# Optimization experiments

Measured on AMD Instinct MI355X. Metric: run time of the kernel, lower is better.

Reference implementation:

```python
import jax, jax.numpy as jnp
import numpy as np

NQ = 4
PI_HALF = np.pi / 2
HAD = jnp.array([[1, 1], [1, -1]], dtype=jnp.complex64) / np.sqrt(2)
CNOT = jnp.array([[1, 0, 0, 0], [0, 1, 0, 0], [0, 0, 0, 1], [0, 0, 1, 0]], dtype=jnp.complex64)
_bits = (np.arange(2 ** NQ)[:, None] >> np.arange(NQ - 1, -1, -1)[None, :]) & 1
ZSIGNS = jnp.asarray(1.0 - 2.0 * _bits, jnp.float32)  # [16, NQ]


def _ry(theta):
    c = jnp.cos(theta / 2).astype(jnp.complex64)
    s = jnp.sin(theta / 2).astype(jnp.complex64)
    return jnp.stack([jnp.stack([c, -s], -1), jnp.stack([s, c], -1)], -2)  # [...,2,2]


def _rot(phi, theta, omega):
    # PennyLane Rot = RZ(omega) @ RY(theta) @ RZ(phi)
    c = jnp.cos(theta / 2).astype(jnp.complex64)
    s = jnp.sin(theta / 2).astype(jnp.complex64)
    ep = jnp.exp(0.5j * phi).astype(jnp.complex64)
    eo = jnp.exp(0.5j * omega).astype(jnp.complex64)
    return jnp.stack([jnp.stack([jnp.conj(ep) * jnp.conj(eo) * c, -ep * jnp.conj(eo) * s]),
                      jnp.stack([jnp.conj(ep) * eo * s, ep * eo * c])])


def _cry(theta):
    # controlled-RY, batched: [B] -> [B,4,4], basis order (control, target)
    B = theta.shape[0]
    U = jnp.zeros((B, 4, 4), jnp.complex64).at[:, 0, 0].set(1.0).at[:, 1, 1].set(1.0)
    return U.at[:, 2:, 2:].set(_ry(theta))


def _apply1(state, U, wire):
    s = jnp.moveaxis(state, wire + 1, 1)
    shp = s.shape
    s = s.reshape(shp[0], 2, -1)
    s = jnp.einsum('ij,bjk->bik', U, s) if U.ndim == 2 else jnp.einsum('bij,bjk->bik', U, s)
    return jnp.moveaxis(s.reshape(shp), 1, wire + 1)


def _apply2(state, U, q0, q1):
    s = jnp.moveaxis(state, (q0 + 1, q1 + 1), (1, 2))
    shp = s.shape
    s = s.reshape(shp[0], 4, -1)
    s = jnp.einsum('ij,bjk->bik', U, s) if U.ndim == 2 else jnp.einsum('bij,bjk->bik', U, s)
    return jnp.moveaxis(s.reshape(shp), (1, 2), (q0 + 1, q1 + 1))


def _init_state(B):
    s = jnp.zeros((B, 2 ** NQ), jnp.complex64).at[:, 0].set(1.0)
    return s.reshape((B,) + (2,) * NQ)


def _zexp(state):
    p = state.reshape(state.shape[0], -1)
    p = p.real ** 2 + p.imag ** 2
    return p @ ZSIGNS  # [B, NQ]


def _attention_circuit(q, k, params):
    # q, k: [E, NQ] angles; params: [NQ, 3] shared
    s = _init_state(q.shape[0])
    for i in range(NQ):
        s = _apply1(s, _ry(q[:, i]), i)
    for i in range(NQ):
        s = _apply1(s, HAD, i)
    for i in range(NQ):
        s = _apply2(s, _cry(k[:, i]), i, (i + 1) % NQ)
    for i in range(NQ):
        s = _apply1(s, _rot(params[i, 0], params[i, 1], params[i, 2]), i)
    return _zexp(s)


def _entangle_circuit(x, params):
    # x: [N, NQ] angles; params: [n_layers, NQ, 3]
    s = _init_state(x.shape[0])
    for i in range(NQ):
        s = _apply1(s, _ry(x[:, i]), i)
    for l in range(params.shape[0]):
        for i in range(NQ - 1):
            s = _apply2(s, CNOT, i, i + 1)
        for i in range(NQ):
            s = _apply1(s, _rot(params[l, i, 0], params[l, i, 1], params[l, i, 2]), i)
        s = _apply2(s, CNOT, 0, NQ - 1)  # n_qubits >= 4
    return _zexp(s)


def _path_circuit(x, params):
    # x: [N, NQ]; params: [3, NQ, 3]
    s = _init_state(x.shape[0])
    for i in range(NQ):
        s = _apply1(s, HAD, i)
    for i in range(NQ):
        s = _apply1(s, _ry(x[:, i]), i)
    for l in range(3):
        for i in range(NQ):
            s = _apply1(s, _rot(params[l, i, 0], params[l, i, 1], params[l, i, 2]), i)
        for i in range(NQ - 1):
            s = _apply2(s, CNOT, i, i + 1)
    return _zexp(s)


def _forward(x, W_in, b_in, lin_W, lin_b, qproj_W, qproj_b, ent_params,
             attq_W, attq_b, attk_W, attk_b, att_qp, path_params,
             path_in_W, path_in_b, path_out_W, path_out_b, out_W, out_b, edge_index):
    N = x.shape[0]
    loops = jnp.arange(N, dtype=edge_index.dtype)
    ei = jnp.concatenate([edge_index, jnp.stack([loops, loops])], axis=1)  # add_self_loops
    src, dst = ei[0], ei[1]
    h = jax.nn.relu(x @ W_in.T + b_in)
    for l in range(lin_W.shape[0]):
        x_cls = h @ lin_W[l].T + lin_b[l]
        xq = _entangle_circuit(jnp.tanh(h[:, :NQ]) * PI_HALF, ent_params[l])
        x_comb = x_cls + xq @ qproj_W[l].T + qproj_b[l]
        q = jnp.tanh(h @ attq_W[l].T + attq_b[l]) * PI_HALF
        k = jnp.tanh(h @ attk_W[l].T + attk_b[l]) * PI_HALF
        scores = _attention_circuit(q[src], k[dst], att_qp[l]).mean(axis=1)  # [E]
        att = jax.nn.softmax(scores)  # global softmax over all edges (faithful)
        h = jax.ops.segment_sum(att[:, None] * x_comb[src], dst, num_segments=N)
        h = jax.nn.relu(h)  # dropout is identity at eval
    pq = jnp.tanh(h @ path_in_W.T + path_in_b) * PI_HALF
    h = _path_circuit(pq, path_params) @ path_out_W.T + path_out_b
    return h @ out_W.T + out_b


def setup_inputs() -> dict:
    key = jax.random.key(0)
    ks = jax.random.split(key, 22)
    N, E, D_in, D_h, D_out, L = 20000, 300000, 64, 128, 32, 2
    w = lambda k, shape: jax.random.normal(k, shape, jnp.float32) * 0.1
    return {
        'x': jax.random.normal(ks[0], (N, D_in), jnp.float32),
        'W_in': w(ks[1], (D_h, D_in)), 'b_in': w(ks[2], (D_h,)),
        'lin_W': w(ks[3], (L, D_h, D_h)), 'lin_b': w(ks[4], (L, D_h)),
        'qproj_W': w(ks[5], (L, D_h, NQ)), 'qproj_b': w(ks[6], (L, D_h)),
        'ent_params': w(ks[7], (L, 2, NQ, 3)),
        'attq_W': w(ks[8], (L, NQ, D_h)), 'attq_b': w(ks[9], (L, NQ)),
        'attk_W': w(ks[10], (L, NQ, D_h)), 'attk_b': w(ks[11], (L, NQ)),
        'att_qp': w(ks[12], (L, NQ, 3)),
        'path_params': w(ks[13], (3, NQ, 3)),
        'path_in_W': w(ks[14], (NQ, D_h)), 'path_in_b': w(ks[15], (NQ,)),
        'path_out_W': w(ks[16], (D_h, NQ)), 'path_out_b': w(ks[17], (D_h,)),
        'out_W': w(ks[18], (D_out, D_h)), 'out_b': w(ks[19], (D_out,)),
        'edge_index': jax.random.randint(ks[20], (2, E), 0, N, dtype=jnp.int32),
    }


def reference(x, W_in, b_in, lin_W, lin_b, qproj_W, qproj_b, ent_params,
              attq_W, attq_b, attk_W, attk_b, att_qp, path_params,
              path_in_W, path_in_b, path_out_W, path_out_b, out_W, out_b, edge_index):
    return _forward(x, W_in, b_in, lin_W, lin_b, qproj_W, qproj_b, ent_params,
                    attq_W, attq_b, attk_W, attk_b, att_qp, path_params,
                    path_in_W, path_in_b, path_out_W, path_out_b, out_W, out_b, edge_index)
```

## Files before the change

kernel.cpp:

```cpp
#include <hip/hip_runtime.h>
#include <math.h>

#define PI_HALF 1.57079632679489662f


__device__ __forceinline__ void init_state(float sr[16], float si[16]) {
#pragma unroll
    for (int i = 0; i < 16; ++i) { sr[i] = 0.f; si[i] = 0.f; }
    sr[0] = 1.f;
}

template<int M>
__device__ __forceinline__ void ry_g(float sr[16], float si[16], float c, float s) {
#pragma unroll
    for (int i = 0; i < 16; ++i) {
        if (i & M) continue;
        const int j = i | M;
        float ar = sr[i], ai = si[i], br = sr[j], bi = si[j];
        sr[i] = c * ar - s * br;  si[i] = c * ai - s * bi;
        sr[j] = s * ar + c * br;  si[j] = s * ai + c * bi;
    }
}

template<int M>
__device__ __forceinline__ void had_g(float sr[16], float si[16]) {
    const float r = 0.70710678118654752f;
#pragma unroll
    for (int i = 0; i < 16; ++i) {
        if (i & M) continue;
        const int j = i | M;
        float ar = sr[i], ai = si[i], br = sr[j], bi = si[j];
        sr[i] = (ar + br) * r;  si[i] = (ai + bi) * r;
        sr[j] = (ar - br) * r;  si[j] = (ai - bi) * r;
    }
}

template<int MC, int MT>
__device__ __forceinline__ void cnot_g(float sr[16], float si[16]) {
#pragma unroll
    for (int i = 0; i < 16; ++i) {
        if (!(i & MC) || (i & MT)) continue;
        const int j = i | MT;
        float tr = sr[i], ti = si[i];
        sr[i] = sr[j]; si[i] = si[j];
        sr[j] = tr;    si[j] = ti;
    }
}

template<int MC, int MT>
__device__ __forceinline__ void cry_g(float sr[16], float si[16], float c, float s) {
#pragma unroll
    for (int i = 0; i < 16; ++i) {
        if (!(i & MC) || (i & MT)) continue;
        const int j = i | MT;
        float ar = sr[i], ai = si[i], br = sr[j], bi = si[j];
        sr[i] = c * ar - s * br;  si[i] = c * ai - s * bi;
        sr[j] = s * ar + c * br;  si[j] = s * ai + c * bi;
    }
}

template<int M>
__device__ __forceinline__ void rot_g(float sr[16], float si[16],
                                      float phi, float theta, float omega) {
    float st, ct; sincosf(0.5f * theta, &st, &ct);
    float sp, cp; sincosf(0.5f * (phi + omega), &sp, &cp);
    float sm, cm; sincosf(0.5f * (phi - omega), &sm, &cm);
    float u00r =  ct * cp, u00i = -ct * sp;
    float u01r = -st * cm, u01i = -st * sm;
    float u10r =  st * cm, u10i = -st * sm;
    float u11r =  ct * cp, u11i =  ct * sp;
#pragma unroll
    for (int i = 0; i < 16; ++i) {
        if (i & M) continue;
        const int j = i | M;
        float ar = sr[i], ai = si[i], br = sr[j], bi = si[j];
        sr[i] = u00r * ar - u00i * ai + u01r * br - u01i * bi;
        si[i] = u00r * ai + u00i * ar + u01r * bi + u01i * br;
        sr[j] = u10r * ar - u10i * ai + u11r * br - u11i * bi;
        si[j] = u10r * ai + u10i * ar + u11r * bi + u11i * br;
    }
}

__device__ __forceinline__ void zexp_g(const float sr[16], const float si[16], float z[4]) {
    float p[16];
#pragma unroll
    for (int i = 0; i < 16; ++i) p[i] = sr[i] * sr[i] + si[i] * si[i];
    z[0] = z[1] = z[2] = z[3] = 0.f;
#pragma unroll
    for (int i = 0; i < 16; ++i) {
        z[0] += (i & 8) ? -p[i] : p[i];
        z[1] += (i & 4) ? -p[i] : p[i];
        z[2] += (i & 2) ? -p[i] : p[i];
        z[3] += (i & 1) ? -p[i] : p[i];
    }
}


__global__ void k_in(const float* __restrict__ x, const float* __restrict__ W,
                     const float* __restrict__ b, float* __restrict__ h, int N) {
    __shared__ float xs[16 * 64];
    const int base = blockIdx.x * 16;
    const int tid = threadIdx.x;
    for (int idx = tid; idx < 16 * 64; idx += 128) {
        int n = base + (idx >> 6);
        xs[idx] = (n < N) ? x[(size_t)n * 64 + (idx & 63)] : 0.f;
    }
    __syncthreads();
    float acc[16];
#pragma unroll
    for (int n = 0; n < 16; ++n) acc[n] = 0.f;
    const float4* wr4 = (const float4*)(W + tid * 64);
    for (int c4 = 0; c4 < 16; ++c4) {
        float4 w = wr4[c4];
#pragma unroll
        for (int n = 0; n < 16; ++n) {
            float4 hv = *(const float4*)&xs[n * 64 + c4 * 4];
            acc[n] += w.x * hv.x + w.y * hv.y + w.z * hv.z + w.w * hv.w;
        }
    }
    const float bb = b[tid];
#pragma unroll
    for (int n = 0; n < 16; ++n) {
        int node = base + n;
        if (node < N) h[(size_t)node * 128 + tid] = fmaxf(acc[n] + bb, 0.f);
    }
}

__global__ void k_ent(const float* __restrict__ h, const float* __restrict__ ep,
                      float* __restrict__ xq, int N) {
    int n = blockIdx.x * blockDim.x + threadIdx.x;
    if (n >= N) return;
    float4 hv = *(const float4*)&h[(size_t)n * 128];
    float a[4] = { tanhf(hv.x) * PI_HALF, tanhf(hv.y) * PI_HALF,
                   tanhf(hv.z) * PI_HALF, tanhf(hv.w) * PI_HALF };
    float sr[16], si[16];
    init_state(sr, si);
    { float s, c; sincosf(0.5f * a[0], &s, &c); ry_g<8>(sr, si, c, s); }
    { float s, c; sincosf(0.5f * a[1], &s, &c); ry_g<4>(sr, si, c, s); }
    { float s, c; sincosf(0.5f * a[2], &s, &c); ry_g<2>(sr, si, c, s); }
    { float s, c; sincosf(0.5f * a[3], &s, &c); ry_g<1>(sr, si, c, s); }
#pragma unroll
    for (int l = 0; l < 2; ++l) {
        cnot_g<8, 4>(sr, si); cnot_g<4, 2>(sr, si); cnot_g<2, 1>(sr, si);
        const float* P = ep + l * 12;
        rot_g<8>(sr, si, P[0], P[1], P[2]);
        rot_g<4>(sr, si, P[3], P[4], P[5]);
        rot_g<2>(sr, si, P[6], P[7], P[8]);
        rot_g<1>(sr, si, P[9], P[10], P[11]);
        cnot_g<8, 1>(sr, si);
    }
    float z[4]; zexp_g(sr, si, z);
    *(float4*)&xq[(size_t)n * 4] = make_float4(z[0], z[1], z[2], z[3]);
}

__global__ void k_lin(const float* __restrict__ h, const float* __restrict__ xq,
                      const float* __restrict__ linW, const float* __restrict__ linb,
                      const float* __restrict__ qpW, const float* __restrict__ qpb,
                      const float* __restrict__ aqW, const float* __restrict__ aqb,
                      const float* __restrict__ akW, const float* __restrict__ akb,
                      float* __restrict__ xcomb, float* __restrict__ qbuf,
                      float* __restrict__ kbuf, int N) {
    __shared__ float hs[16 * 128];
    __shared__ float xqs[16 * 4];
    const int base = blockIdx.x * 16;
    const int tid = threadIdx.x;
    for (int idx = tid; idx < 16 * 128; idx += 128) {
        int n = base + (idx >> 7);
        hs[idx] = (n < N) ? h[(size_t)n * 128 + (idx & 127)] : 0.f;
    }
    if (tid < 64) {
        int n = base + (tid >> 2);
        xqs[tid] = (n < N) ? xq[(size_t)n * 4 + (tid & 3)] : 0.f;
    }
    __syncthreads();
    float acc[16];
#pragma unroll
    for (int n = 0; n < 16; ++n) acc[n] = 0.f;
    const float4* wr4 = (const float4*)(linW + tid * 128);
    for (int c4 = 0; c4 < 32; ++c4) {
        float4 w = wr4[c4];
#pragma unroll
        for (int n = 0; n < 16; ++n) {
            float4 hv = *(const float4*)&hs[n * 128 + c4 * 4];
            acc[n] += w.x * hv.x + w.y * hv.y + w.z * hv.z + w.w * hv.w;
        }
    }
    const float bb = linb[tid] + qpb[tid];
    const float qw0 = qpW[tid * 4 + 0], qw1 = qpW[tid * 4 + 1];
    const float qw2 = qpW[tid * 4 + 2], qw3 = qpW[tid * 4 + 3];
#pragma unroll
    for (int n = 0; n < 16; ++n) {
        int node = base + n;
        if (node < N) {
            xcomb[(size_t)node * 128 + tid] = acc[n] + bb
                + qw0 * xqs[n * 4 + 0] + qw1 * xqs[n * 4 + 1]
                + qw2 * xqs[n * 4 + 2] + qw3 * xqs[n * 4 + 3];
        }
    }
    const int nl = tid >> 3;
    const int which = tid & 7;
    const int qi = which & 3;
    const float4* Wp4 = (const float4*)(((which < 4) ? aqW : akW) + qi * 128);
    float dot = (which < 4) ? aqb[qi] : akb[qi];
    for (int c4 = 0; c4 < 32; ++c4) {
        float4 w = Wp4[c4];
        float4 hv = *(const float4*)&hs[nl * 128 + c4 * 4];
        dot += w.x * hv.x + w.y * hv.y + w.z * hv.z + w.w * hv.w;
    }
    int node = base + nl;
    if (node < N) {
        float val = tanhf(dot) * PI_HALF;
        if (which < 4) qbuf[(size_t)node * 4 + qi] = val;
        else           kbuf[(size_t)node * 4 + qi] = val;
    }
}

__global__ void k_att(const float* __restrict__ qb, const float* __restrict__ kb,
                      const int* __restrict__ ei, const float* __restrict__ P,
                      float* __restrict__ scores, float* __restrict__ sumexp,
                      int E, int EP) {
    __shared__ float red[256];
    int e = blockIdx.x * blockDim.x + threadIdx.x;
    float ex = 0.f;
    if (e < EP) {
        int s_, d_;
        if (e < E) { s_ = ei[e]; d_ = ei[E + e]; } else { s_ = d_ = e - E; }
        float4 q = *(const float4*)&qb[(size_t)s_ * 4];
        float4 k = *(const float4*)&kb[(size_t)d_ * 4];
        float sr[16], si[16];
        init_state(sr, si);
        { float s, c; sincosf(0.5f * q.x, &s, &c); ry_g<8>(sr, si, c, s); }
        { float s, c; sincosf(0.5f * q.y, &s, &c); ry_g<4>(sr, si, c, s); }
        { float s, c; sincosf(0.5f * q.z, &s, &c); ry_g<2>(sr, si, c, s); }
        { float s, c; sincosf(0.5f * q.w, &s, &c); ry_g<1>(sr, si, c, s); }
        had_g<8>(sr, si); had_g<4>(sr, si); had_g<2>(sr, si); had_g<1>(sr, si);
        { float s, c; sincosf(0.5f * k.x, &s, &c); cry_g<8, 4>(sr, si, c, s); }
        { float s, c; sincosf(0.5f * k.y, &s, &c); cry_g<4, 2>(sr, si, c, s); }
        { float s, c; sincosf(0.5f * k.z, &s, &c); cry_g<2, 1>(sr, si, c, s); }
        { float s, c; sincosf(0.5f * k.w, &s, &c); cry_g<1, 8>(sr, si, c, s); }
        rot_g<8>(sr, si, P[0], P[1], P[2]);
        rot_g<4>(sr, si, P[3], P[4], P[5]);
        rot_g<2>(sr, si, P[6], P[7], P[8]);
        rot_g<1>(sr, si, P[9], P[10], P[11]);
        float z[4]; zexp_g(sr, si, z);
        float sc = 0.25f * (z[0] + z[1] + z[2] + z[3]);
        scores[e] = sc;
        ex = expf(sc);
    }
    red[threadIdx.x] = ex;
    __syncthreads();
    for (int s = 128; s > 0; s >>= 1) {
        if ((int)threadIdx.x < s) red[threadIdx.x] += red[threadIdx.x + s];
        __syncthreads();
    }
    if (threadIdx.x == 0) atomicAdd(sumexp, red[0]);
}


__global__ void k_hist(const int* __restrict__ ei, int* __restrict__ cnt, int E, int EP) {
    int e = blockIdx.x * blockDim.x + threadIdx.x;
    if (e >= EP) return;
    int d_ = (e < E) ? ei[E + e] : e - E;
    atomicAdd(&cnt[d_], 1);
}

__global__ void k_scan(const int* __restrict__ cnt, int* __restrict__ off,
                       int* __restrict__ cur, int N) {
    __shared__ int tot[1024];
    const int t = threadIdx.x;
    const int chunk = (N + 1023) >> 10;
    const int s0 = t * chunk;
    const int s1 = min(s0 + chunk, N);
    int sum = 0;
    for (int i = s0; i < s1; ++i) sum += cnt[i];
    tot[t] = sum;
    __syncthreads();
    for (int d = 1; d < 1024; d <<= 1) {
        int v = (t >= d) ? tot[t - d] : 0;
        __syncthreads();
        tot[t] += v;
        __syncthreads();
    }
    int run = (t == 0) ? 0 : tot[t - 1];
    for (int i = s0; i < s1; ++i) {
        off[i] = run; cur[i] = run;
        run += cnt[i];
    }
}

__global__ void k_fill(const int* __restrict__ ei, int* __restrict__ cur,
                       int* __restrict__ srcs, int* __restrict__ eids, int E, int EP) {
    int e = blockIdx.x * blockDim.x + threadIdx.x;
    if (e >= EP) return;
    int s_, d_;
    if (e < E) { s_ = ei[e]; d_ = ei[E + e]; } else { s_ = d_ = e - E; }
    int pos = atomicAdd(&cur[d_], 1);
    srcs[pos] = s_;
    eids[pos] = e;
}

__global__ void k_wexp(const float* __restrict__ scores, const int* __restrict__ eids,
                       const float* __restrict__ sumexp, float* __restrict__ watt, int EP) {
    int t = blockIdx.x * blockDim.x + threadIdx.x;
    if (t >= EP) return;
    watt[t] = expf(scores[eids[t]]) / sumexp[0];
}

__global__ void k_gather(const float* __restrict__ xcomb, const int* __restrict__ srcs,
                         const float* __restrict__ watt, const int* __restrict__ off,
                         const int* __restrict__ cnt, float* __restrict__ h) {
    __shared__ int sS[128];
    __shared__ float wS[128];
    const int b = blockIdx.x;
    const int tid = threadIdx.x;
    const int start = off[b];
    const int num = cnt[b];
    float acc = 0.f;
    for (int base = 0; base < num; base += 128) {
        int m = min(128, num - base);
        if (tid < m) {
            sS[tid] = srcs[start + base + tid];
            wS[tid] = watt[start + base + tid];
        }
        __syncthreads();
        for (int i = 0; i < m; ++i)
            acc += wS[i] * xcomb[(size_t)sS[i] * 128 + tid];
        __syncthreads();
    }
    h[(size_t)b * 128 + tid] = fmaxf(acc, 0.f);
}

__global__ void k_fusemat(const float* __restrict__ outW, const float* __restrict__ outb,
                          const float* __restrict__ poW, const float* __restrict__ pob,
                          float* __restrict__ M, float* __restrict__ v) {
    int t = threadIdx.x;
    if (t < 128) {
        int o = t >> 2, i = t & 3;
        float acc = 0.f;
        for (int j = 0; j < 128; ++j) acc += outW[o * 128 + j] * poW[j * 4 + i];
        M[t] = acc;
    } else if (t < 160) {
        int o = t - 128;
        float acc = outb[o];
        for (int j = 0; j < 128; ++j) acc += outW[o * 128 + j] * pob[j];
        v[o] = acc;
    }
}

#define PQ_STRIDE 132
__global__ void k_pq(const float* __restrict__ h, const float* __restrict__ piW,
                     const float* __restrict__ pib, float* __restrict__ pq, int N) {
    __shared__ float hs[32 * PQ_STRIDE];
    const int base = blockIdx.x * 32;
    const int tid = threadIdx.x;
    for (int idx = tid; idx < 32 * 128; idx += 128) {
        int n = base + (idx >> 7);
        hs[(idx >> 7) * PQ_STRIDE + (idx & 127)] = (n < N) ? h[(size_t)n * 128 + (idx & 127)] : 0.f;
    }
    __syncthreads();
    const int nl = tid >> 2;
    const int i  = tid & 3;
    float dot = pib[i];
    const float4* w4 = (const float4*)(piW + i * 128);
    for (int c4 = 0; c4 < 32; ++c4) {
        float4 w = w4[c4];
        float4 hv = *(const float4*)&hs[nl * PQ_STRIDE + c4 * 4];
        dot += w.x * hv.x + w.y * hv.y + w.z * hv.z + w.w * hv.w;
    }
    int node = base + nl;
    if (node < N) pq[(size_t)node * 4 + i] = tanhf(dot) * PI_HALF;
}

__global__ void k_pathc(const float* __restrict__ pq, const float* __restrict__ pp,
                        const float* __restrict__ M, const float* __restrict__ v,
                        float* __restrict__ out, int N) {
    __shared__ float zS[256 * 4];
    __shared__ float MS[128];
    __shared__ float vS[32];
    __shared__ float ppS[36];
    const int tid = threadIdx.x;
    if (tid < 128) MS[tid] = M[tid];
    else if (tid < 160) vS[tid - 128] = v[tid - 128];
    else if (tid < 196) ppS[tid - 160] = pp[tid - 160];
    __syncthreads();
    const int base = blockIdx.x * 256;
    const int n = base + tid;
    if (n < N) {
        float4 a = *(const float4*)&pq[(size_t)n * 4];
        float sr[16], si[16];
        init_state(sr, si);
        had_g<8>(sr, si); had_g<4>(sr, si); had_g<2>(sr, si); had_g<1>(sr, si);
        { float s, c; sincosf(0.5f * a.x, &s, &c); ry_g<8>(sr, si, c, s); }
        { float s, c; sincosf(0.5f * a.y, &s, &c); ry_g<4>(sr, si, c, s); }
        { float s, c; sincosf(0.5f * a.z, &s, &c); ry_g<2>(sr, si, c, s); }
        { float s, c; sincosf(0.5f * a.w, &s, &c); ry_g<1>(sr, si, c, s); }
#pragma unroll
        for (int l = 0; l < 3; ++l) {
            const float* P = ppS + l * 12;
            rot_g<8>(sr, si, P[0], P[1], P[2]);
            rot_g<4>(sr, si, P[3], P[4], P[5]);
            rot_g<2>(sr, si, P[6], P[7], P[8]);
            rot_g<1>(sr, si, P[9], P[10], P[11]);
            cnot_g<8, 4>(sr, si); cnot_g<4, 2>(sr, si); cnot_g<2, 1>(sr, si);
        }
        float z[4]; zexp_g(sr, si, z);
        zS[tid * 4 + 0] = z[0]; zS[tid * 4 + 1] = z[1];
        zS[tid * 4 + 2] = z[2]; zS[tid * 4 + 3] = z[3];
    }
    __syncthreads();
#pragma unroll
    for (int k = 0; k < 32; ++k) {
        int flat = k * 256 + tid;
        int nl = flat >> 5;
        int o = flat & 31;
        int node = base + nl;
        if (node < N) {
            out[(size_t)node * 32 + o] = vS[o]
                + MS[o * 4 + 0] * zS[nl * 4 + 0] + MS[o * 4 + 1] * zS[nl * 4 + 1]
                + MS[o * 4 + 2] * zS[nl * 4 + 2] + MS[o * 4 + 3] * zS[nl * 4 + 3];
        }
    }
}


extern "C" void kernel_launch(void* const* d_in, const int* in_sizes, int n_in,
                              void* d_out, int out_size, void* d_ws, size_t ws_size,
                              hipStream_t stream) {
    const float* x     = (const float*)d_in[0];
    const float* W_in  = (const float*)d_in[1];
    const float* b_in  = (const float*)d_in[2];
    const float* linW  = (const float*)d_in[3];
    const float* linb  = (const float*)d_in[4];
    const float* qpW   = (const float*)d_in[5];
    const float* qpb   = (const float*)d_in[6];
    const float* entp  = (const float*)d_in[7];
    const float* aqW   = (const float*)d_in[8];
    const float* aqb   = (const float*)d_in[9];
    const float* akW   = (const float*)d_in[10];
    const float* akb   = (const float*)d_in[11];
    const float* attqp = (const float*)d_in[12];
    const float* pparm = (const float*)d_in[13];
    const float* piW   = (const float*)d_in[14];
    const float* pib   = (const float*)d_in[15];
    const float* poW   = (const float*)d_in[16];
    const float* pob   = (const float*)d_in[17];
    const float* outW  = (const float*)d_in[18];
    const float* outb  = (const float*)d_in[19];
    const int*   ei    = (const int*)d_in[20];

    const int N  = in_sizes[0] / 64;
    const int E  = in_sizes[20] / 2;
    const int EP = E + N;

    float* ws     = (float*)d_ws;
    float* h      = ws;
    float* xcomb  = h      + (size_t)N * 128;
    float* xq     = xcomb  + (size_t)N * 128;
    float* qbuf   = xq     + (size_t)N * 4;
    float* kbuf   = qbuf   + (size_t)N * 4;
    float* pq     = kbuf   + (size_t)N * 4;
    float* scores = pq     + (size_t)N * 4;
    float* watt   = scores + EP;
    float* sumexp = watt   + EP;
    float* Mm     = sumexp + 4;
    float* vv     = Mm + 128;
    int*   cnt    = (int*)(vv + 32);
    int*   off    = cnt + N;
    int*   cur    = off + N;
    int*   srcs   = cur + N;
    int*   eids   = srcs + EP;

    const int nb16 = (N + 15) / 16;
    const int ebl  = (EP + 255) / 256;

    hipMemsetAsync(cnt, 0, (size_t)N * sizeof(int), stream);
    k_hist<<<ebl, 256, 0, stream>>>(ei, cnt, E, EP);
    k_scan<<<1, 1024, 0, stream>>>(cnt, off, cur, N);
    k_fill<<<ebl, 256, 0, stream>>>(ei, cur, srcs, eids, E, EP);

    k_in<<<nb16, 128, 0, stream>>>(x, W_in, b_in, h, N);

    for (int l = 0; l < 2; ++l) {
        k_ent<<<(N + 255) / 256, 256, 0, stream>>>(h, entp + l * 24, xq, N);
        k_lin<<<nb16, 128, 0, stream>>>(h, xq,
            linW + (size_t)l * 128 * 128, linb + l * 128,
            qpW + (size_t)l * 128 * 4, qpb + l * 128,
            aqW + (size_t)l * 4 * 128, aqb + l * 4,
            akW + (size_t)l * 4 * 128, akb + l * 4,
            xcomb, qbuf, kbuf, N);
        hipMemsetAsync(sumexp, 0, sizeof(float), stream);
        k_att<<<ebl, 256, 0, stream>>>(qbuf, kbuf, ei, attqp + l * 12,
                                       scores, sumexp, E, EP);
        k_wexp<<<ebl, 256, 0, stream>>>(scores, eids, sumexp, watt, EP);
        k_gather<<<N, 128, 0, stream>>>(xcomb, srcs, watt, off, cnt, h);
    }

    k_fusemat<<<1, 192, 0, stream>>>(outW, outb, poW, pob, Mm, vv);
    k_pq<<<(N + 31) / 32, 128, 0, stream>>>(h, piW, pib, pq, N);
    k_pathc<<<(N + 255) / 256, 256, 0, stream>>>(pq, pparm, Mm, vv, (float*)d_out, N);
}
```

Measured before the change: 425.0 us.

## Precompute rotation matrices, fuse softmax normalization into gather, use fast math

Adds a setup kernel that computes all shared Rot gate matrices once and folds in the output matrix fusion, so the circuit kernels no longer evaluate sincos per gate per thread. k_lin and k_pq now store cos/sin of the half angles instead of the angles, and tanh/sincos switch to fast intrinsics. The k_wexp kernel is removed: k_att writes exp(score) straight into CSR order through an inverse permutation, and k_gather divides by the sum at the end. A single memset covers both sumexp slots. This saves launches and transcendental work at some cost in precision from the fast intrinsics.

```diff
diff --git a/kernel.cpp b/kernel.cpp
--- a/kernel.cpp
+++ b/kernel.cpp
@@ -2,6 +2,11 @@
 #include <math.h>
 
 #define PI_HALF 1.57079632679489662f
+
+__device__ __forceinline__ float fast_tanh(float x) {
+    float e = __expf(2.f * x);
+    return 1.f - 2.f * __builtin_amdgcn_rcpf(e + 1.f);
+}
 
 
 __device__ __forceinline__ void init_state(float sr[16], float si[16]) {
@@ -60,15 +65,9 @@
 }
 
 template<int M>
-__device__ __forceinline__ void rot_g(float sr[16], float si[16],
-                                      float phi, float theta, float omega) {
-    float st, ct; sincosf(0.5f * theta, &st, &ct);
-    float sp, cp; sincosf(0.5f * (phi + omega), &sp, &cp);
-    float sm, cm; sincosf(0.5f * (phi - omega), &sm, &cm);
-    float u00r =  ct * cp, u00i = -ct * sp;
-    float u01r = -st * cm, u01i = -st * sm;
-    float u10r =  st * cm, u10i = -st * sm;
-    float u11r =  ct * cp, u11i =  ct * sp;
+__device__ __forceinline__ void rot_pre(float sr[16], float si[16], const float* __restrict__ u) {
+    const float u00r = u[0], u00i = u[1], u01r = u[2], u01i = u[3];
+    const float u10r = u[4], u10i = u[5], u11r = u[6], u11i = u[7];
 #pragma unroll
     for (int i = 0; i < 16; ++i) {
         if (i & M) continue;
@@ -95,6 +94,41 @@
     }
 }
 
+__global__ void k_setup(const float* __restrict__ entp, const float* __restrict__ attqp,
+                        const float* __restrict__ pparm,
+                        const float* __restrict__ outW, const float* __restrict__ outb,
+                        const float* __restrict__ poW, const float* __restrict__ pob,
+                        float* __restrict__ rotbuf, float* __restrict__ M,
+                        float* __restrict__ v) {
+    const int t = threadIdx.x;
+    if (t < 36) {
+        const float* p;
+        if (t < 16)      p = entp  + t * 3;
+        else if (t < 24) p = attqp + (t - 16) * 3;
+        else             p = pparm + (t - 24) * 3;
+        float phi = p[0], theta = p[1], omega = p[2];
+        float st, ct; sincosf(0.5f * theta, &st, &ct);
+        float sp, cp; sincosf(0.5f * (phi + omega), &sp, &cp);
+        float sm, cm; sincosf(0.5f * (phi - omega), &sm, &cm);
+        float* u = rotbuf + t * 8;
+        u[0] =  ct * cp;  u[1] = -ct * sp;
+        u[2] = -st * cm;  u[3] = -st * sm;
+        u[4] =  st * cm;  u[5] = -st * sm;
+        u[6] =  ct * cp;  u[7] =  ct * sp;
+    } else if (t >= 64 && t < 192) {
+        int t2 = t - 64;
+        int o = t2 >> 2, i = t2 & 3;
+        float acc = 0.f;
+        for (int j = 0; j < 128; ++j) acc += outW[o * 128 + j] * poW[j * 4 + i];
+        M[t2] = acc;
+    } else if (t >= 192 && t < 224) {
+        int o = t - 192;
+        float acc = outb[o];
+        for (int j = 0; j < 128; ++j) acc += outW[o * 128 + j] * pob[j];
+        v[o] = acc;
+    }
+}
+
 
 __global__ void k_in(const float* __restrict__ x, const float* __restrict__ W,
                      const float* __restrict__ b, float* __restrict__ h, int N) {
@@ -126,27 +160,25 @@
     }
 }
 
-__global__ void k_ent(const float* __restrict__ h, const float* __restrict__ ep,
+__global__ void k_ent(const float* __restrict__ h, const float* __restrict__ rotE,
                       float* __restrict__ xq, int N) {
     int n = blockIdx.x * blockDim.x + threadIdx.x;
     if (n >= N) return;
     float4 hv = *(const float4*)&h[(size_t)n * 128];
-    float a[4] = { tanhf(hv.x) * PI_HALF, tanhf(hv.y) * PI_HALF,
-                   tanhf(hv.z) * PI_HALF, tanhf(hv.w) * PI_HALF };
     float sr[16], si[16];
     init_state(sr, si);
-    { float s, c; sincosf(0.5f * a[0], &s, &c); ry_g<8>(sr, si, c, s); }
-    { float s, c; sincosf(0.5f * a[1], &s, &c); ry_g<4>(sr, si, c, s); }
-    { float s, c; sincosf(0.5f * a[2], &s, &c); ry_g<2>(sr, si, c, s); }
-    { float s, c; sincosf(0.5f * a[3], &s, &c); ry_g<1>(sr, si, c, s); }
+    { float s, c; __sincosf(fast_tanh(hv.x) * (0.5f * PI_HALF), &s, &c); ry_g<8>(sr, si, c, s); }
+    { float s, c; __sincosf(fast_tanh(hv.y) * (0.5f * PI_HALF), &s, &c); ry_g<4>(sr, si, c, s); }
+    { float s, c; __sincosf(fast_tanh(hv.z) * (0.5f * PI_HALF), &s, &c); ry_g<2>(sr, si, c, s); }
+    { float s, c; __sincosf(fast_tanh(hv.w) * (0.5f * PI_HALF), &s, &c); ry_g<1>(sr, si, c, s); }
 #pragma unroll
     for (int l = 0; l < 2; ++l) {
         cnot_g<8, 4>(sr, si); cnot_g<4, 2>(sr, si); cnot_g<2, 1>(sr, si);
-        const float* P = ep + l * 12;
-        rot_g<8>(sr, si, P[0], P[1], P[2]);
-        rot_g<4>(sr, si, P[3], P[4], P[5]);
-        rot_g<2>(sr, si, P[6], P[7], P[8]);
-        rot_g<1>(sr, si, P[9], P[10], P[11]);
+        const float* P = rotE + l * 32;
+        rot_pre<8>(sr, si, P);
+        rot_pre<4>(sr, si, P + 8);
+        rot_pre<2>(sr, si, P + 16);
+        rot_pre<1>(sr, si, P + 24);
         cnot_g<8, 1>(sr, si);
     }
     float z[4]; zexp_g(sr, si, z);
@@ -209,43 +241,46 @@
     }
     int node = base + nl;
     if (node < N) {
-        float val = tanhf(dot) * PI_HALF;
-        if (which < 4) qbuf[(size_t)node * 4 + qi] = val;
-        else           kbuf[(size_t)node * 4 + qi] = val;
+        float half = fast_tanh(dot) * (0.5f * PI_HALF);
+        float s, c; __sincosf(half, &s, &c);
+        float* dst = ((which < 4) ? qbuf : kbuf) + (size_t)node * 8 + qi * 2;
+        dst[0] = c; dst[1] = s;
     }
 }
 
 __global__ void k_att(const float* __restrict__ qb, const float* __restrict__ kb,
-                      const int* __restrict__ ei, const float* __restrict__ P,
-                      float* __restrict__ scores, float* __restrict__ sumexp,
-                      int E, int EP) {
+                      const int* __restrict__ ei, const float* __restrict__ RA,
+                      const int* __restrict__ inv, float* __restrict__ escore,
+                      float* __restrict__ sumexp, int E, int EP) {
     __shared__ float red[256];
     int e = blockIdx.x * blockDim.x + threadIdx.x;
     float ex = 0.f;
     if (e < EP) {
         int s_, d_;
         if (e < E) { s_ = ei[e]; d_ = ei[E + e]; } else { s_ = d_ = e - E; }
-        float4 q = *(const float4*)&qb[(size_t)s_ * 4];
-        float4 k = *(const float4*)&kb[(size_t)d_ * 4];
+        float4 qa = *(const float4*)&qb[(size_t)s_ * 8];
+        float4 qc = *(const float4*)&qb[(size_t)s_ * 8 + 4];
+        float4 ka = *(const float4*)&kb[(size_t)d_ * 8];
+        float4 kc = *(const float4*)&kb[(size_t)d_ * 8 + 4];
         float sr[16], si[16];
         init_state(sr, si);
-        { float s, c; sincosf(0.5f * q.x, &s, &c); ry_g<8>(sr, si, c, s); }
-        { float s, c; sincosf(0.5f * q.y, &s, &c); ry_g<4>(sr, si, c, s); }
-        { float s, c; sincosf(0.5f * q.z, &s, &c); ry_g<2>(sr, si, c, s); }
-        { float s, c; sincosf(0.5f * q.w, &s, &c); ry_g<1>(sr, si, c, s); }
+        ry_g<8>(sr, si, qa.x, qa.y);
+        ry_g<4>(sr, si, qa.z, qa.w);
+        ry_g<2>(sr, si, qc.x, qc.y);
+        ry_g<1>(sr, si, qc.z, qc.w);
         had_g<8>(sr, si); had_g<4>(sr, si); had_g<2>(sr, si); had_g<1>(sr, si);
-        { float s, c; sincosf(0.5f * k.x, &s, &c); cry_g<8, 4>(sr, si, c, s); }
-        { float s, c; sincosf(0.5f * k.y, &s, &c); cry_g<4, 2>(sr, si, c, s); }
-        { float s, c; sincosf(0.5f * k.z, &s, &c); cry_g<2, 1>(sr, si, c, s); }
-        { float s, c; sincosf(0.5f * k.w, &s, &c); cry_g<1, 8>(sr, si, c, s); }
-        rot_g<8>(sr, si, P[0], P[1], P[2]);
-        rot_g<4>(sr, si, P[3], P[4], P[5]);
-        rot_g<2>(sr, si, P[6], P[7], P[8]);
-        rot_g<1>(sr, si, P[9], P[10], P[11]);
+        cry_g<8, 4>(sr, si, ka.x, ka.y);
+        cry_g<4, 2>(sr, si, ka.z, ka.w);
+        cry_g<2, 1>(sr, si, kc.x, kc.y);
+        cry_g<1, 8>(sr, si, kc.z, kc.w);
+        rot_pre<8>(sr, si, RA);
+        rot_pre<4>(sr, si, RA + 8);
+        rot_pre<2>(sr, si, RA + 16);
+        rot_pre<1>(sr, si, RA + 24);
         float z[4]; zexp_g(sr, si, z);
         float sc = 0.25f * (z[0] + z[1] + z[2] + z[3]);
-        scores[e] = sc;
-        ex = expf(sc);
+        ex = __expf(sc);
+        escore[inv[e]] = ex;
     }
     red[threadIdx.x] = ex;
     __syncthreads();
@@ -289,26 +324,20 @@
 }
 
 __global__ void k_fill(const int* __restrict__ ei, int* __restrict__ cur,
-                       int* __restrict__ srcs, int* __restrict__ eids, int E, int EP) {
+                       int* __restrict__ srcs, int* __restrict__ inv, int E, int EP) {
     int e = blockIdx.x * blockDim.x + threadIdx.x;
     if (e >= EP) return;
     int s_, d_;
     if (e < E) { s_ = ei[e]; d_ = ei[E + e]; } else { s_ = d_ = e - E; }
     int pos = atomicAdd(&cur[d_], 1);
     srcs[pos] = s_;
-    eids[pos] = e;
-}
-
-__global__ void k_wexp(const float* __restrict__ scores, const int* __restrict__ eids,
-                       const float* __restrict__ sumexp, float* __restrict__ watt, int EP) {
-    int t = blockIdx.x * blockDim.x + threadIdx.x;
-    if (t >= EP) return;
-    watt[t] = expf(scores[eids[t]]) / sumexp[0];
+    inv[e] = pos;
 }
 
 __global__ void k_gather(const float* __restrict__ xcomb, const int* __restrict__ srcs,
-                         const float* __restrict__ watt, const int* __restrict__ off,
-                         const int* __restrict__ cnt, float* __restrict__ h) {
+                         const float* __restrict__ escore, const int* __restrict__ off,
+                         const int* __restrict__ cnt, const float* __restrict__ sumexp,
+                         float* __restrict__ h) {
     __shared__ int sS[128];
     __shared__ float wS[128];
     const int b = blockIdx.x;
@@ -320,36 +349,20 @@
         int m = min(128, num - base);
         if (tid < m) {
             sS[tid] = srcs[start + base + tid];
-            wS[tid] = watt[start + base + tid];
+            wS[tid] = escore[start + base + tid];
         }
         __syncthreads();
         for (int i = 0; i < m; ++i)
             acc += wS[i] * xcomb[(size_t)sS[i] * 128 + tid];
         __syncthreads();
     }
-    h[(size_t)b * 128 + tid] = fmaxf(acc, 0.f);
-}
-
-__global__ void k_fusemat(const float* __restrict__ outW, const float* __restrict__ outb,
-                          const float* __restrict__ poW, const float* __restrict__ pob,
-                          float* __restrict__ M, float* __restrict__ v) {
-    int t = threadIdx.x;
-    if (t < 128) {
-        int o = t >> 2, i = t & 3;
-        float acc = 0.f;
-        for (int j = 0; j < 128; ++j) acc += outW[o * 128 + j] * poW[j * 4 + i];
-        M[t] = acc;
-    } else if (t < 160) {
-        int o = t - 128;
-        float acc = outb[o];
-        for (int j = 0; j < 128; ++j) acc += outW[o * 128 + j] * pob[j];
-        v[o] = acc;
-    }
+    const float invS = __builtin_amdgcn_rcpf(sumexp[0]);
+    h[(size_t)b * 128 + tid] = fmaxf(acc * invS, 0.f);
 }
 
 #define PQ_STRIDE 132
 __global__ void k_pq(const float* __restrict__ h, const float* __restrict__ piW,
-                     const float* __restrict__ pib, float* __restrict__ pq, int N) {
+                     const float* __restrict__ pib, float* __restrict__ pq8, int N) {
     __shared__ float hs[32 * PQ_STRIDE];
     const int base = blockIdx.x * 32;
     const int tid = threadIdx.x;
@@ -368,39 +381,43 @@
         dot += w.x * hv.x + w.y * hv.y + w.z * hv.z + w.w * hv.w;
     }
     int node = base + nl;
-    if (node < N) pq[(size_t)node * 4 + i] = tanhf(dot) * PI_HALF;
-}
-
-__global__ void k_pathc(const float* __restrict__ pq, const float* __restrict__ pp,
+    if (node < N) {
+        float half = fast_tanh(dot) * (0.5f * PI_HALF);
+        float s, c; __sincosf(half, &s, &c);
+        pq8[(size_t)node * 8 + i * 2]     = c;
+        pq8[(size_t)node * 8 + i * 2 + 1] = s;
+    }
+}
+
+__global__ void k_pathc(const float* __restrict__ pq8, const float* __restrict__ RP,
                         const float* __restrict__ M, const float* __restrict__ v,
                         float* __restrict__ out, int N) {
     __shared__ float zS[256 * 4];
     __shared__ float MS[128];
     __shared__ float vS[32];
-    __shared__ float ppS[36];
     const int tid = threadIdx.x;
     if (tid < 128) MS[tid] = M[tid];
     else if (tid < 160) vS[tid - 128] = v[tid - 128];
-    else if (tid < 196) ppS[tid - 160] = pp[tid - 160];
     __syncthreads();
     const int base = blockIdx.x * 256;
     const int n = base + tid;
     if (n < N) {
-        float4 a = *(const float4*)&pq[(size_t)n * 4];
+        float4 pa = *(const float4*)&pq8[(size_t)n * 8];
+        float4 pc = *(const float4*)&pq8[(size_t)n * 8 + 4];
         float sr[16], si[16];
         init_state(sr, si);
         had_g<8>(sr, si); had_g<4>(sr, si); had_g<2>(sr, si); had_g<1>(sr, si);
-        { float s, c; sincosf(0.5f * a.x, &s, &c); ry_g<8>(sr, si, c, s); }
-        { float s, c; sincosf(0.5f * a.y, &s, &c); ry_g<4>(sr, si, c, s); }
-        { float s, c; sincosf(0.5f * a.z, &s, &c); ry_g<2>(sr, si, c, s); }
-        { float s, c; sincosf(0.5f * a.w, &s, &c); ry_g<1>(sr, si, c, s); }
+        ry_g<8>(sr, si, pa.x, pa.y);
+        ry_g<4>(sr, si, pa.z, pa.w);
+        ry_g<2>(sr, si, pc.x, pc.y);
+        ry_g<1>(sr, si, pc.z, pc.w);
 #pragma unroll
         for (int l = 0; l < 3; ++l) {
-            const float* P = ppS + l * 12;
-            rot_g<8>(sr, si, P[0], P[1], P[2]);
-            rot_g<4>(sr, si, P[3], P[4], P[5]);
-            rot_g<2>(sr, si, P[6], P[7], P[8]);
-            rot_g<1>(sr, si, P[9], P[10], P[11]);
+            const float* P = RP + l * 32;
+            rot_pre<8>(sr, si, P);
+            rot_pre<4>(sr, si, P + 8);
+            rot_pre<2>(sr, si, P + 16);
+            rot_pre<1>(sr, si, P + 24);
             cnot_g<8, 4>(sr, si); cnot_g<4, 2>(sr, si); cnot_g<2, 1>(sr, si);
         }
         float z[4]; zexp_g(sr, si, z);
@@ -457,45 +474,47 @@
     float* xcomb  = h      + (size_t)N * 128;
     float* xq     = xcomb  + (size_t)N * 128;
     float* qbuf   = xq     + (size_t)N * 4;
-    float* kbuf   = qbuf   + (size_t)N * 4;
-    float* pq     = kbuf   + (size_t)N * 4;
-    float* scores = pq     + (size_t)N * 4;
-    float* watt   = scores + EP;
-    float* sumexp = watt   + EP;
-    float* Mm     = sumexp + 4;
+    float* kbuf   = qbuf   + (size_t)N * 8;
+    float* pq8    = kbuf   + (size_t)N * 8;
+    float* escore = pq8    + (size_t)N * 8;
+    float* rotbuf = escore + EP;
+    float* Mm     = rotbuf + 36 * 8;
     float* vv     = Mm + 128;
     int*   cnt    = (int*)(vv + 32);
-    int*   off    = cnt + N;
+    float* sumexp = (float*)(cnt + N);
+    int*   off    = (int*)(sumexp + 4);
     int*   cur    = off + N;
     int*   srcs   = cur + N;
-    int*   eids   = srcs + EP;
+    int*   inv    = srcs + EP;
+
+    const float* rotE = rotbuf;
+    const float* rotA = rotbuf + 128;
+    const float* rotP = rotbuf + 192;
 
     const int nb16 = (N + 15) / 16;
     const int ebl  = (EP + 255) / 256;
 
-    hipMemsetAsync(cnt, 0, (size_t)N * sizeof(int), stream);
+    hipMemsetAsync(cnt, 0, (size_t)(N + 4) * sizeof(int), stream);
     k_hist<<<ebl, 256, 0, stream>>>(ei, cnt, E, EP);
     k_scan<<<1, 1024, 0, stream>>>(cnt, off, cur, N);
-    k_fill<<<ebl, 256, 0, stream>>>(ei, cur, srcs, eids, E, EP);
-
+    k_fill<<<ebl, 256, 0, stream>>>(ei, cur, srcs, inv, E, EP);
+    k_setup<<<1, 256, 0, stream>>>(entp, attqp, pparm, outW, outb, poW, pob,
+                                   rotbuf, Mm, vv);
     k_in<<<nb16, 128, 0, stream>>>(x, W_in, b_in, h, N);
 
     for (int l = 0; l < 2; ++l) {
-        k_ent<<<(N + 255) / 256, 256, 0, stream>>>(h, entp + l * 24, xq, N);
+        k_ent<<<(N + 255) / 256, 256, 0, stream>>>(h, rotE + l * 64, xq, N);
         k_lin<<<nb16, 128, 0, stream>>>(h, xq,
             linW + (size_t)l * 128 * 128, linb + l * 128,
             qpW + (size_t)l * 128 * 4, qpb + l * 128,
             aqW + (size_t)l * 4 * 128, aqb + l * 4,
             akW + (size_t)l * 4 * 128, akb + l * 4,
             xcomb, qbuf, kbuf, N);
-        hipMemsetAsync(sumexp, 0, sizeof(float), stream);
-        k_att<<<ebl, 256, 0, stream>>>(qbuf, kbuf, ei, attqp + l * 12,
-                                       scores, sumexp, E, EP);
-        k_wexp<<<ebl, 256, 0, stream>>>(scores, eids, sumexp, watt, EP);
-        k_gather<<<N, 128, 0, stream>>>(xcomb, srcs, watt, off, cnt, h);
-    }
-
-    k_fusemat<<<1, 192, 0, stream>>>(outW, outb, poW, pob, Mm, vv);
-    k_pq<<<(N + 31) / 32, 128, 0, stream>>>(h, piW, pib, pq, N);
-    k_pathc<<<(N + 255) / 256, 256, 0, stream>>>(pq, pparm, Mm, vv, (float*)d_out, N);
-}
+        k_att<<<ebl, 256, 0, stream>>>(qbuf, kbuf, ei, rotA + l * 32, inv,
+                                       escore, sumexp + l, E, EP);
+        k_gather<<<N, 128, 0, stream>>>(xcomb, srcs, escore, off, cnt, sumexp + l, h);
+    }
+
+    k_pq<<<(N + 31) / 32, 128, 0, stream>>>(h, piW, pib, pq8, N);
+    k_pathc<<<(N + 255) / 256, 256, 0, stream>>>(pq8, rotP, Mm, vv, (float*)d_out, N);
+}
```

After: 397.0 us. 1.07x faster.
